# Performance work log

Hardware: AMD Instinct MI355X
Metric: run time of the kernel (lower is better)

Reference implementation:

```python
import jax, jax.numpy as jnp
import numpy as np

D_MODEL = 1024
NUM_HEADS = 16
HEAD_DIM = D_MODEL // NUM_HEADS


def setup_inputs() -> dict:
    key = jax.random.key(0)
    ks = jax.random.split(key, 11)
    B, S, D = 2, 2048, D_MODEL
    scale = 1.0 / np.sqrt(D)
    inp = {
        "query": jax.random.normal(ks[0], (B, S, D), jnp.float32),
        "key": jax.random.normal(ks[1], (B, S, D), jnp.float32),
        "value": jax.random.normal(ks[2], (B, S, D), jnp.float32),
        "Wq": jax.random.normal(ks[3], (D, D), jnp.float32) * scale,
        "bq": jnp.zeros((D,), jnp.float32),
        "Wk": jax.random.normal(ks[4], (D, D), jnp.float32) * scale,
        "bk": jnp.zeros((D,), jnp.float32),
        "Wv": jax.random.normal(ks[5], (D, D), jnp.float32) * scale,
        "bv": jnp.zeros((D,), jnp.float32),
        "Wo": jax.random.normal(ks[6], (D, D), jnp.float32) * scale,
        "bo": jnp.zeros((D,), jnp.float32),
    }
    return inp


def reference(query, key, value, Wq, bq, Wk, bk, Wv, bv, Wo, bo):
    B, S, D = query.shape
    H, hd = NUM_HEADS, HEAD_DIM
    # linear projections (x @ W^T + b, torch nn.Linear convention)
    Q = query @ Wq.T + bq
    K = key @ Wk.T + bk
    V = value @ Wv.T + bv
    # split heads: [B, S, H, hd] -> [B, H, S, hd]
    Q = Q.reshape(B, S, H, hd).transpose(0, 2, 1, 3)
    K = K.reshape(B, S, H, hd).transpose(0, 2, 1, 3)
    V = V.reshape(B, S, H, hd).transpose(0, 2, 1, 3)
    # scaled dot-product attention (explicit, non-flash)
    scores = jnp.einsum("bhqd,bhkd->bhqk", Q, K) / jnp.sqrt(jnp.float32(hd)).astype(Q.dtype)
    attn = jax.nn.softmax(scores, axis=-1)
    out = jnp.einsum("bhqk,bhkd->bhqd", attn, V)
    # merge heads: [B, H, S, hd] -> [B, S, D]
    out = out.transpose(0, 2, 1, 3).reshape(B, S, D)
    return out @ Wo.T + bo
```

## Files before the change

### kernel.cpp

```cpp
#include <hip/hip_runtime.h>
#include <hip/hip_bf16.h>


constexpr int D_MODEL = 1024;
constexpr int S_LEN   = 2048;
constexpr int BATCH   = 2;
constexpr int NH      = 16;
constexpr int HD      = 64;
constexpr int ROWS    = BATCH * S_LEN;

typedef __attribute__((ext_vector_type(8))) short short8;
typedef __attribute__((ext_vector_type(4))) float float4a;

static __device__ __forceinline__ unsigned short f2bf(float f) {
  union { float f; unsigned u; } v{f};
  unsigned r = v.u + 0x7FFFu + ((v.u >> 16) & 1u);
  return (unsigned short)(r >> 16);
}

static __device__ __forceinline__ unsigned pack_bf16(float a, float b) {
#if __has_builtin(__builtin_amdgcn_cvt_pk_bf16_f32)
  typedef __attribute__((ext_vector_type(2))) __bf16 bf16x2;
  union { bf16x2 v; unsigned u; } c;
  c.v = __builtin_amdgcn_cvt_pk_bf16_f32(a, b);
  return c.u;
#else
  return (unsigned)f2bf(a) | ((unsigned)f2bf(b) << 16);
#endif
}

static __device__ __forceinline__ float bf2f(unsigned short u) {
  union { unsigned u; float f; } v;
  v.u = (unsigned)u << 16;
  return v.f;
}

static __device__ __forceinline__ void async16(const void* g, void* l) {
  __builtin_amdgcn_global_load_lds(
      (const __attribute__((address_space(1))) unsigned int*)g,
      (__attribute__((address_space(3))) unsigned int*)l, 16, 0, 0);
}

struct ConvArgs { const float* s[7]; unsigned short* d[7]; int n[7]; };

__global__ __launch_bounds__(256) void convert_bf16(ConvArgs a) {
  const int which = blockIdx.y;
  const int i = (blockIdx.x * 256 + threadIdx.x) * 8;
  if (i >= a.n[which]) return;
  const float4* s = (const float4*)(a.s[which] + i);
  float4 x = s[0], y = s[1];
  unsigned t[4] = {pack_bf16(x.x, x.y), pack_bf16(x.z, x.w),
                   pack_bf16(y.x, y.y), pack_bf16(y.z, y.w)};
  *(short8*)(a.d[which] + i) = *(short8*)t;
}

template <int MODE>
static __device__ __forceinline__ void gemm_body(
    const unsigned short* __restrict__ A, const unsigned short* __restrict__ W,
    const float* __restrict__ bias, void* __restrict__ Yv, float scale,
    unsigned short* As, unsigned short* Bs, unsigned short* Tb) {
  const int tid = threadIdx.x;
  const int w = tid >> 6, lane = tid & 63;
  const int l15 = lane & 15, quad = lane >> 4;
  const int row0 = blockIdx.x * 128, col0 = blockIdx.y * 128;
  const int wm = (w & 1) * 64, wn = (w >> 1) * 64;

  float4a acc[4][4];
#pragma unroll
  for (int i = 0; i < 4; i++)
#pragma unroll
    for (int j = 0; j < 4; j++) acc[i][j] = (float4a){0.f, 0.f, 0.f, 0.f};

  for (int kt = 0; kt < D_MODEL; kt += 64) {
    __syncthreads();
#pragma unroll
    for (int j = 0; j < 4; j++) {
      const int i = w * 4 + j;
      const int r = i * 8 + (lane >> 3);
      const int c = ((lane & 7) - (r >> 1)) & 7;
      async16(W + (size_t)(col0 + r) * D_MODEL + kt + c * 8, (char*)Bs + i * 1024);
      async16(A + (size_t)(row0 + r) * D_MODEL + kt + c * 8, (char*)As + i * 1024);
    }
    __syncthreads();

#pragma unroll
    for (int kk = 0; kk < 2; kk++) {
      const int sw = (kk * 4 + quad + (l15 >> 1)) & 7;
      short8 af[4], bf[4];
#pragma unroll
      for (int mt = 0; mt < 4; mt++) {
        const int r = wm + mt * 16 + l15;
        af[mt] = *(const short8*)&As[(r * 8 + sw) * 8];
      }
#pragma unroll
      for (int nt = 0; nt < 4; nt++) {
        const int r = wn + nt * 16 + l15;
        bf[nt] = *(const short8*)&Bs[(r * 8 + sw) * 8];
      }
#pragma unroll
      for (int mt = 0; mt < 4; mt++)
#pragma unroll
        for (int nt = 0; nt < 4; nt++)
          acc[mt][nt] = __builtin_amdgcn_mfma_f32_16x16x32_bf16(af[mt], bf[nt], acc[mt][nt], 0, 0, 0);
    }
  }

  int cols[4];
  float bvs[4];
#pragma unroll
  for (int nt = 0; nt < 4; nt++) {
    cols[nt] = col0 + wn + nt * 16 + l15;
    bvs[nt]  = bias[cols[nt]] * ((MODE == 0) ? scale : 1.0f);
  }

  if constexpr (MODE == 0) {
    unsigned short* Y = (unsigned short*)Yv;
#pragma unroll
    for (int mt = 0; mt < 4; mt++)
#pragma unroll
      for (int r = 0; r < 4; r++) {
        const int m = row0 + wm + mt * 16 + quad * 4 + r;
        const int bb = m >> 11, s = m & 2047;
#pragma unroll
        for (int nt = 0; nt < 4; nt++) {
          const int h = cols[nt] >> 6, d = cols[nt] & 63;
          Y[(((size_t)(bb * NH + h)) * S_LEN + s) * HD + d] =
              f2bf(acc[mt][nt][r] * scale + bvs[nt]);
        }
      }
  } else {
    __syncthreads();
    unsigned short* T = Tb + w * (64 * 32);
    unsigned short* Y = (unsigned short*)Yv;
#pragma unroll
    for (int p = 0; p < 2; p++) {
      if (p) { asm volatile("s_waitcnt lgkmcnt(0)" ::: "memory"); }
#pragma unroll
      for (int mi = 0; mi < 2; mi++) {
        const int mt = 2 * p + mi;
#pragma unroll
        for (int r = 0; r < 4; r++) {
          const int sl = mi * 16 + quad * 4 + r;
          const int cch = sl >> 3;
#pragma unroll
          for (int nt = 0; nt < 4; nt++) {
            const int dl = nt * 16 + l15;
            const int slot = cch ^ (dl & 3);
            T[dl * 32 + slot * 8 + (sl & 7)] = f2bf(acc[mt][nt][r] + bvs[nt]);
          }
        }
      }
      asm volatile("s_waitcnt lgkmcnt(0)" ::: "memory");
#pragma unroll
      for (int j = 0; j < 4; j++) {
        const int cid = j * 64 + lane;
        const int dl = cid >> 2;
        const int c  = cid & 3;
        const int slot = c ^ (dl & 3);
        short8 v = *(const short8*)&T[dl * 32 + slot * 8];
        const int col = col0 + wn + dl;
        const int h = col >> 6, d = col & 63;
        const int m = row0 + wm + p * 32 + c * 8;
        const int bb = m >> 11, s = m & 2047;
        *(short8*)&Y[(((size_t)(bb * NH + h)) * HD + d) * S_LEN + s] = v;
      }
    }
  }
}

__global__ __launch_bounds__(256) void gemm_qkv(
    const unsigned short* xq, const unsigned short* xk, const unsigned short* xv,
    const unsigned short* wq, const unsigned short* wk, const unsigned short* wv,
    const float* bq, const float* bk, const float* bv,
    unsigned short* Q, unsigned short* K, unsigned short* Vt) {
  __shared__ unsigned short smem[2 * 128 * 64];
  unsigned short* As = smem;
  unsigned short* Bs = smem + 128 * 64;
  unsigned short* Tb = smem;
  const int z = blockIdx.z;
  if (z == 0)      gemm_body<0>(xq, wq, bq, Q,  0.125f * 1.44269504f, As, Bs, Tb);
  else if (z == 1) gemm_body<0>(xk, wk, bk, K,  1.0f, As, Bs, Tb);
  else             gemm_body<2>(xv, wv, bv, Vt, 1.0f, As, Bs, Tb);
}

__global__ __launch_bounds__(256) void gemm_o(
    const unsigned short* __restrict__ Op, const float* __restrict__ Lp,
    const unsigned short* __restrict__ wo, const float* __restrict__ bo,
    float* __restrict__ out) {
  __shared__ unsigned short As[64 * 64];
  __shared__ unsigned short Bs[128 * 64];
  const int tid = threadIdx.x;
  const int w = tid >> 6, lane = tid & 63;
  const int l15 = lane & 15, quad = lane >> 4;
  const int row0 = blockIdx.x * 64, col0 = blockIdx.y * 128;
  const int wn = w * 32;

  const int ar = w * 16 + (lane >> 2);
  const int cg = lane & 3;
  const int asl0 = (cg + (ar >> 1)) & 7;
  const int asl1 = (cg + 4 + (ar >> 1)) & 7;
  const int grow = row0 + ar;
  const unsigned short* P0 = Op + (size_t)grow * D_MODEL + cg * 8;
  const unsigned short* P1 = P0 + (size_t)ROWS * D_MODEL;
  const float* L0 = Lp + (size_t)grow * NH;
  const float* L1 = L0 + (size_t)ROWS * NH;

  float4a acc[4][2];
#pragma unroll
  for (int i = 0; i < 4; i++)
#pragma unroll
    for (int j = 0; j < 2; j++) acc[i][j] = (float4a){0.f, 0.f, 0.f, 0.f};

  for (int kt = 0; kt < D_MODEL; kt += 64) {
    const int h = kt >> 6;
    const float rinv = 1.0f / (L0[h] + L1[h]);
    short8 a0 = *(const short8*)(P0 + kt);
    short8 a1 = *(const short8*)(P0 + kt + 32);
    short8 b0 = *(const short8*)(P1 + kt);
    short8 b1 = *(const short8*)(P1 + kt + 32);
    unsigned t0[4], t1[4];
#pragma unroll
    for (int i = 0; i < 4; i++) {
      const float u0 = (bf2f((unsigned short)a0[2 * i]) + bf2f((unsigned short)b0[2 * i])) * rinv;
      const float u1 = (bf2f((unsigned short)a0[2 * i + 1]) + bf2f((unsigned short)b0[2 * i + 1])) * rinv;
      t0[i] = pack_bf16(u0, u1);
      const float v0 = (bf2f((unsigned short)a1[2 * i]) + bf2f((unsigned short)b1[2 * i])) * rinv;
      const float v1 = (bf2f((unsigned short)a1[2 * i + 1]) + bf2f((unsigned short)b1[2 * i + 1])) * rinv;
      t1[i] = pack_bf16(v0, v1);
    }
    __syncthreads();
    *(short8*)&As[(ar * 8 + asl0) * 8] = *(short8*)t0;
    *(short8*)&As[(ar * 8 + asl1) * 8] = *(short8*)t1;
#pragma unroll
    for (int j = 0; j < 4; j++) {
      const int i = w * 4 + j;
      const int r = i * 8 + (lane >> 3);
      const int c = ((lane & 7) - (r >> 1)) & 7;
      async16(wo + (size_t)(col0 + r) * D_MODEL + kt + c * 8, (char*)Bs + i * 1024);
    }
    __syncthreads();

#pragma unroll
    for (int kk = 0; kk < 2; kk++) {
      const int sw = (kk * 4 + quad + (l15 >> 1)) & 7;
      short8 af[4], bf[2];
#pragma unroll
      for (int mt = 0; mt < 4; mt++) {
        const int r = mt * 16 + l15;
        af[mt] = *(const short8*)&As[(r * 8 + sw) * 8];
      }
#pragma unroll
      for (int nt = 0; nt < 2; nt++) {
        const int r = wn + nt * 16 + l15;
        bf[nt] = *(const short8*)&Bs[(r * 8 + sw) * 8];
      }
#pragma unroll
      for (int mt = 0; mt < 4; mt++)
#pragma unroll
        for (int nt = 0; nt < 2; nt++)
          acc[mt][nt] = __builtin_amdgcn_mfma_f32_16x16x32_bf16(af[mt], bf[nt], acc[mt][nt], 0, 0, 0);
    }
  }

#pragma unroll
  for (int nt = 0; nt < 2; nt++) {
    const int col = col0 + wn + nt * 16 + l15;
    const float bv = bo[col];
#pragma unroll
    for (int mt = 0; mt < 4; mt++)
#pragma unroll
      for (int r = 0; r < 4; r++) {
        const int m = row0 + mt * 16 + quad * 4 + r;
        out[(size_t)m * D_MODEL + col] = acc[mt][nt][r] + bv;
      }
  }
}

__global__ __launch_bounds__(256) void attn_kernel(
    const unsigned short* __restrict__ Qh, const unsigned short* __restrict__ Kh,
    const unsigned short* __restrict__ Vt, unsigned short* __restrict__ Op,
    float* __restrict__ Lp) {
  const int n   = blockIdx.x;
  const int idx = n >> 3;
  const int qb  = idx & 15;
  const int g   = (n & 7) + 8 * (idx >> 4);
  const int h   = g & 15;
  const int z   = g >> 4;
  const int bb  = z >> 1, sp = z & 1;

  const int tid = threadIdx.x;
  const int w = tid >> 6, lane = tid & 63;
  const int l15 = lane & 15, quad = lane >> 4;

  __shared__ unsigned short Ks[64 * 64];
  __shared__ unsigned short Vs[64 * 64];
  __shared__ unsigned short Ps[4][32][72];

  const size_t bh = (size_t)(bb * NH + h);
  const unsigned short* Qp = Qh + bh * S_LEN * HD;
  const unsigned short* Kp = Kh + bh * S_LEN * HD;
  const unsigned short* Vp = Vt + bh * (size_t)HD * S_LEN;

  const int r0 = w * 16 + (lane >> 3);
  const int c0 = ((lane & 7) - r0) & 7;
  const unsigned short* Kg0 = Kp + (size_t)r0 * HD + c0 * 8;
  const unsigned short* Kg1 = Kg0 + 8 * HD;
  const unsigned short* Vg0 = Vp + (size_t)r0 * S_LEN + c0 * 8;
  const unsigned short* Vg1 = Vg0 + 8 * S_LEN;
  unsigned short* Kd0 = (unsigned short*)((char*)Ks + (w * 2) * 1024 + (size_t)lane * 16);
  unsigned short* Kd1 = (unsigned short*)((char*)Kd0 + 1024);
  unsigned short* Vd0 = (unsigned short*)((char*)Vs + (w * 2) * 1024 + (size_t)lane * 16);
  unsigned short* Vd1 = (unsigned short*)((char*)Vd0 + 1024);

  short8 qf[2][2];
#pragma unroll
  for (int qnt = 0; qnt < 2; qnt++)
#pragma unroll
    for (int c = 0; c < 2; c++)
      qf[qnt][c] = *(const short8*)(Qp + (size_t)(qb * 128 + w * 32 + qnt * 16 + l15) * HD +
                                    c * 32 + quad * 8);

  unsigned short ob[8] = {0x3F80, 0x3F80, 0x3F80, 0x3F80, 0x3F80, 0x3F80, 0x3F80, 0x3F80};
  const short8 ones = *(short8*)ob;

  float4a Oacc[2][4];
#pragma unroll
  for (int a = 0; a < 2; a++)
#pragma unroll
    for (int b = 0; b < 4; b++) Oacc[a][b] = (float4a){0.f, 0.f, 0.f, 0.f};
  float4a Lacc[2] = {(float4a){0.f, 0.f, 0.f, 0.f}, (float4a){0.f, 0.f, 0.f, 0.f}};

  const int sw0 = (quad + l15) & 7;
  const int sw1 = (quad + 4 + l15) & 7;

  const int kb0 = sp * 1024, kbend = kb0 + 1024;

  short8 kr0 = *(const short8*)(Kg0 + (size_t)kb0 * HD);
  short8 kr1 = *(const short8*)(Kg1 + (size_t)kb0 * HD);
  short8 vr0 = *(const short8*)(Vg0 + kb0);
  short8 vr1 = *(const short8*)(Vg1 + kb0);

  for (int kb = kb0; kb < kbend; kb += 64) {
    asm volatile("s_waitcnt lgkmcnt(0)" ::: "memory");
    __builtin_amdgcn_sched_barrier(0);
    __builtin_amdgcn_s_barrier();
    asm volatile("s_waitcnt vmcnt(0)" ::: "memory");
    __builtin_amdgcn_sched_barrier(0);
    *(short8*)Kd0 = kr0;
    *(short8*)Kd1 = kr1;
    *(short8*)Vd0 = vr0;
    *(short8*)Vd1 = vr1;
    if (kb + 64 < kbend) {
      kr0 = *(const short8*)(Kg0 + (size_t)(kb + 64) * HD);
      kr1 = *(const short8*)(Kg1 + (size_t)(kb + 64) * HD);
      vr0 = *(const short8*)(Vg0 + (kb + 64));
      vr1 = *(const short8*)(Vg1 + (kb + 64));
    }
    asm volatile("s_waitcnt lgkmcnt(0)" ::: "memory");
    __builtin_amdgcn_sched_barrier(0);
    __builtin_amdgcn_s_barrier();

#pragma unroll
    for (int mt = 0; mt < 4; mt++) {
      const int rb = (mt * 16 + l15) * 8;
      short8 a0 = *(const short8*)&Ks[(rb + sw0) * 8];
      short8 a1 = *(const short8*)&Ks[(rb + sw1) * 8];
#pragma unroll
      for (int qnt = 0; qnt < 2; qnt++) {
        float4a s = (float4a){0.f, 0.f, 0.f, 0.f};
        s = __builtin_amdgcn_mfma_f32_16x16x32_bf16(a0, qf[qnt][0], s, 0, 0, 0);
        s = __builtin_amdgcn_mfma_f32_16x16x32_bf16(a1, qf[qnt][1], s, 0, 0, 0);
        uint2 pk;
        pk.x = pack_bf16(__builtin_amdgcn_exp2f(s[0]), __builtin_amdgcn_exp2f(s[1]));
        pk.y = pack_bf16(__builtin_amdgcn_exp2f(s[2]), __builtin_amdgcn_exp2f(s[3]));
        *(uint2*)&Ps[w][qnt * 16 + l15][mt * 16 + quad * 4] = pk;
      }
    }
    asm volatile("s_waitcnt lgkmcnt(0)" ::: "memory");

#pragma unroll
    for (int c = 0; c < 2; c++) {
      short8 pa0 = *(const short8*)&Ps[w][l15][c * 32 + quad * 8];
      short8 pa1 = *(const short8*)&Ps[w][16 + l15][c * 32 + quad * 8];
      Lacc[0] = __builtin_amdgcn_mfma_f32_16x16x32_bf16(pa0, ones, Lacc[0], 0, 0, 0);
      Lacc[1] = __builtin_amdgcn_mfma_f32_16x16x32_bf16(pa1, ones, Lacc[1], 0, 0, 0);
      const int vsw = (c * 4 + quad + l15) & 7;
#pragma unroll
      for (int nt = 0; nt < 4; nt++) {
        short8 vb = *(const short8*)&Vs[((nt * 16 + l15) * 8 + vsw) * 8];
        Oacc[0][nt] = __builtin_amdgcn_mfma_f32_16x16x32_bf16(pa0, vb, Oacc[0][nt], 0, 0, 0);
        Oacc[1][nt] = __builtin_amdgcn_mfma_f32_16x16x32_bf16(pa1, vb, Oacc[1][nt], 0, 0, 0);
      }
    }
  }

  if (l15 == 0) {
#pragma unroll
    for (int qnt = 0; qnt < 2; qnt++)
#pragma unroll
      for (int reg = 0; reg < 4; reg++) {
        const int q = qb * 128 + w * 32 + qnt * 16 + quad * 4 + reg;
        Lp[(size_t)sp * ROWS * NH + ((size_t)bb * S_LEN + q) * NH + h] = Lacc[qnt][reg];
      }
  }

  unsigned short* Ob = Op + (size_t)sp * ROWS * D_MODEL;
#pragma unroll
  for (int qnt = 0; qnt < 2; qnt++) {
#pragma unroll
    for (int reg = 0; reg < 4; reg++) {
      const int q = qb * 128 + w * 32 + qnt * 16 + quad * 4 + reg;
      unsigned short* orow = Ob + ((size_t)bb * S_LEN + q) * D_MODEL + h * HD;
#pragma unroll
      for (int nt = 0; nt < 4; nt++)
        orow[nt * 16 + l15] = f2bf(Oacc[qnt][nt][reg]);
    }
  }
}

extern "C" void kernel_launch(void* const* d_in, const int* in_sizes, int n_in,
                              void* d_out, int out_size, void* d_ws, size_t ws_size,
                              hipStream_t stream) {
  const float* query = (const float*)d_in[0];
  const float* key   = (const float*)d_in[1];
  const float* value = (const float*)d_in[2];
  const float* Wq = (const float*)d_in[3];
  const float* bq = (const float*)d_in[4];
  const float* Wk = (const float*)d_in[5];
  const float* bk = (const float*)d_in[6];
  const float* Wv = (const float*)d_in[7];
  const float* bv = (const float*)d_in[8];
  const float* Wo = (const float*)d_in[9];
  const float* bo = (const float*)d_in[10];
  float* out = (float*)d_out;

  char* ws = (char*)d_ws;
  const size_t MB = 1024 * 1024;
  unsigned short* xq16 = (unsigned short*)(ws + 0 * MB);
  unsigned short* xk16 = (unsigned short*)(ws + 8 * MB);
  unsigned short* xv16 = (unsigned short*)(ws + 16 * MB);
  unsigned short* wq16 = (unsigned short*)(ws + 24 * MB);
  unsigned short* wk16 = (unsigned short*)(ws + 26 * MB);
  unsigned short* wv16 = (unsigned short*)(ws + 28 * MB);
  unsigned short* qbuf  = (unsigned short*)(ws + 32 * MB);
  unsigned short* kbuf  = (unsigned short*)(ws + 40 * MB);
  unsigned short* vtbuf = (unsigned short*)(ws + 48 * MB);
  unsigned short* wo16  = (unsigned short*)(ws + 56 * MB);
  float* Lp = (float*)(ws + 58 * MB);
  unsigned short* Op = (unsigned short*)(ws + 0 * MB);

  ConvArgs ca;
  const int NX = ROWS * D_MODEL, NW = D_MODEL * D_MODEL;
  ca.s[0] = query; ca.d[0] = xq16; ca.n[0] = NX;
  ca.s[1] = key;   ca.d[1] = xk16; ca.n[1] = NX;
  ca.s[2] = value; ca.d[2] = xv16; ca.n[2] = NX;
  ca.s[3] = Wq;    ca.d[3] = wq16; ca.n[3] = NW;
  ca.s[4] = Wk;    ca.d[4] = wk16; ca.n[4] = NW;
  ca.s[5] = Wv;    ca.d[5] = wv16; ca.n[5] = NW;
  ca.s[6] = Wo;    ca.d[6] = wo16; ca.n[6] = NW;
  hipLaunchKernelGGL(convert_bf16, dim3(NX / 2048, 7), dim3(256), 0, stream, ca);

  dim3 gqkv(ROWS / 128, D_MODEL / 128, 3);
  hipLaunchKernelGGL(gemm_qkv, gqkv, dim3(256), 0, stream,
                     xq16, xk16, xv16, wq16, wk16, wv16, bq, bk, bv,
                     qbuf, kbuf, vtbuf);

  hipLaunchKernelGGL(attn_kernel, dim3(1024), dim3(256), 0, stream,
                     qbuf, kbuf, vtbuf, Op, Lp);

  dim3 go(ROWS / 64, D_MODEL / 128);
  hipLaunchKernelGGL(gemm_o, go, dim3(256), 0, stream, Op, Lp, wo16, bo, out);
}
```

Before: 232.3 us.

## Fuse activation fp32-to-bf16 conversion into QKV GEMM and double-buffer weight tiles

The QKV GEMM now reads fp32 activations directly, converts them to bf16 in registers and writes them to LDS, so the separate conversion pass over the three activation tensors and its round trip through memory are gone. Weight tiles in both the QKV and output GEMMs are double-buffered in LDS, with the next tile's async loads issued before the MFMAs of the current tile. This uses more LDS and registers (prefetched fp32 A values), which may lower occupancy, and each QKV block now reads twice as many activation bytes as the bf16 version did.

```diff
diff --git a/kernel.cpp b/kernel.cpp
--- a/kernel.cpp
+++ b/kernel.cpp
@@ -41,7 +41,17 @@
       (__attribute__((address_space(3))) unsigned int*)l, 16, 0, 0);
 }
 
-struct ConvArgs { const float* s[7]; unsigned short* d[7]; int n[7]; };
+#define WAIT_LGKM0_SB() do { \
+  asm volatile("s_waitcnt lgkmcnt(0)" ::: "memory"); \
+  __builtin_amdgcn_sched_barrier(0); } while (0)
+#define WAIT_VM0_SB() do { \
+  asm volatile("s_waitcnt vmcnt(0)" ::: "memory"); \
+  __builtin_amdgcn_sched_barrier(0); } while (0)
+#define BARRIER_SB() do { \
+  __builtin_amdgcn_s_barrier(); \
+  __builtin_amdgcn_sched_barrier(0); } while (0)
+
+struct ConvArgs { const float* s[4]; unsigned short* d[4]; int n[4]; };
 
 __global__ __launch_bounds__(256) void convert_bf16(ConvArgs a) {
   const int which = blockIdx.y;
@@ -56,32 +66,69 @@
 
 template <int MODE>
 static __device__ __forceinline__ void gemm_body(
-    const unsigned short* __restrict__ A, const unsigned short* __restrict__ W,
+    const float* __restrict__ A, const unsigned short* __restrict__ W,
     const float* __restrict__ bias, void* __restrict__ Yv, float scale,
-    unsigned short* As, unsigned short* Bs, unsigned short* Tb) {
+    unsigned short* As, unsigned short* Bsb, unsigned short* Tb) {
   const int tid = threadIdx.x;
   const int w = tid >> 6, lane = tid & 63;
   const int l15 = lane & 15, quad = lane >> 4;
   const int row0 = blockIdx.x * 128, col0 = blockIdx.y * 128;
   const int wm = (w & 1) * 64, wn = (w >> 1) * 64;
 
-  float4a acc[4][4];
-#pragma unroll
-  for (int i = 0; i < 4; i++)
-#pragma unroll
-    for (int j = 0; j < 4; j++) acc[i][j] = (float4a){0.f, 0.f, 0.f, 0.f};
-
-  for (int kt = 0; kt < D_MODEL; kt += 64) {
-    __syncthreads();
+  int rA[4], cA[4];
+#pragma unroll
+  for (int j = 0; j < 4; j++) {
+    const int i = w * 4 + j;
+    rA[j] = i * 8 + (lane >> 3);
+    cA[j] = ((lane & 7) - (rA[j] >> 1)) & 7;
+  }
+
+  float4 av[4][2];
+  auto loadA = [&](int kt) {
+#pragma unroll
+    for (int j = 0; j < 4; j++) {
+      const float* s = A + (size_t)(row0 + rA[j]) * D_MODEL + kt + cA[j] * 8;
+      av[j][0] = *(const float4*)s;
+      av[j][1] = *(const float4*)(s + 4);
+    }
+  };
+  auto loadW = [&](int kt, unsigned short* Bdst) {
 #pragma unroll
     for (int j = 0; j < 4; j++) {
       const int i = w * 4 + j;
-      const int r = i * 8 + (lane >> 3);
-      const int c = ((lane & 7) - (r >> 1)) & 7;
-      async16(W + (size_t)(col0 + r) * D_MODEL + kt + c * 8, (char*)Bs + i * 1024);
-      async16(A + (size_t)(row0 + r) * D_MODEL + kt + c * 8, (char*)As + i * 1024);
-    }
-    __syncthreads();
+      async16(W + (size_t)(col0 + rA[j]) * D_MODEL + kt + cA[j] * 8,
+              (char*)Bdst + i * 1024);
+    }
+  };
+
+  float4a acc[4][4];
+#pragma unroll
+  for (int i = 0; i < 4; i++)
+#pragma unroll
+    for (int j = 0; j < 4; j++) acc[i][j] = (float4a){0.f, 0.f, 0.f, 0.f};
+
+  loadA(0);
+  loadW(0, Bsb);
+
+  for (int kt = 0; kt < D_MODEL; kt += 64) {
+    const int cur = (kt >> 6) & 1;
+    unsigned short* Bc = Bsb + cur * (128 * 64);
+    unsigned short* Bn = Bsb + (cur ^ 1) * (128 * 64);
+    const bool more = (kt + 64 < D_MODEL);
+
+    WAIT_LGKM0_SB();
+    BARRIER_SB();
+    WAIT_VM0_SB();
+#pragma unroll
+    for (int j = 0; j < 4; j++) {
+      unsigned t[4] = {pack_bf16(av[j][0].x, av[j][0].y), pack_bf16(av[j][0].z, av[j][0].w),
+                       pack_bf16(av[j][1].x, av[j][1].y), pack_bf16(av[j][1].z, av[j][1].w)};
+      *(short8*)((char*)As + (w * 4 + j) * 1024 + (size_t)lane * 16) = *(short8*)t;
+    }
+    if (more) loadA(kt + 64);
+    WAIT_LGKM0_SB();
+    BARRIER_SB();
+    if (more) loadW(kt + 64, Bn);
 
 #pragma unroll
     for (int kk = 0; kk < 2; kk++) {
@@ -95,7 +142,7 @@
 #pragma unroll
       for (int nt = 0; nt < 4; nt++) {
         const int r = wn + nt * 16 + l15;
-        bf[nt] = *(const short8*)&Bs[(r * 8 + sw) * 8];
+        bf[nt] = *(const short8*)&Bc[(r * 8 + sw) * 8];
       }
 #pragma unroll
       for (int mt = 0; mt < 4; mt++)
@@ -169,18 +216,18 @@
 }
 
 __global__ __launch_bounds__(256) void gemm_qkv(
-    const unsigned short* xq, const unsigned short* xk, const unsigned short* xv,
+    const float* xq, const float* xk, const float* xv,
     const unsigned short* wq, const unsigned short* wk, const unsigned short* wv,
     const float* bq, const float* bk, const float* bv,
     unsigned short* Q, unsigned short* K, unsigned short* Vt) {
-  __shared__ unsigned short smem[2 * 128 * 64];
-  unsigned short* As = smem;
-  unsigned short* Bs = smem + 128 * 64;
-  unsigned short* Tb = smem;
+  __shared__ unsigned short smem[3 * 128 * 64];
+  unsigned short* As  = smem;
+  unsigned short* Bsb = smem + 128 * 64;
+  unsigned short* Tb  = smem;
   const int z = blockIdx.z;
-  if (z == 0)      gemm_body<0>(xq, wq, bq, Q,  0.125f * 1.44269504f, As, Bs, Tb);
-  else if (z == 1) gemm_body<0>(xk, wk, bk, K,  1.0f, As, Bs, Tb);
-  else             gemm_body<2>(xv, wv, bv, Vt, 1.0f, As, Bs, Tb);
+  if (z == 0)      gemm_body<0>(xq, wq, bq, Q,  0.125f * 1.44269504f, As, Bsb, Tb);
+  else if (z == 1) gemm_body<0>(xk, wk, bk, K,  1.0f, As, Bsb, Tb);
+  else             gemm_body<2>(xv, wv, bv, Vt, 1.0f, As, Bsb, Tb);
 }
 
 __global__ __launch_bounds__(256) void gemm_o(
@@ -188,7 +235,7 @@
     const unsigned short* __restrict__ wo, const float* __restrict__ bo,
     float* __restrict__ out) {
   __shared__ unsigned short As[64 * 64];
-  __shared__ unsigned short Bs[128 * 64];
+  __shared__ unsigned short Bsb[2 * 128 * 64];
   const int tid = threadIdx.x;
   const int w = tid >> 6, lane = tid & 63;
   const int l15 = lane & 15, quad = lane >> 4;
@@ -205,40 +252,71 @@
   const float* L0 = Lp + (size_t)grow * NH;
   const float* L1 = L0 + (size_t)ROWS * NH;
 
-  float4a acc[4][2];
-#pragma unroll
-  for (int i = 0; i < 4; i++)
-#pragma unroll
-    for (int j = 0; j < 2; j++) acc[i][j] = (float4a){0.f, 0.f, 0.f, 0.f};
-
-  for (int kt = 0; kt < D_MODEL; kt += 64) {
-    const int h = kt >> 6;
-    const float rinv = 1.0f / (L0[h] + L1[h]);
-    short8 a0 = *(const short8*)(P0 + kt);
-    short8 a1 = *(const short8*)(P0 + kt + 32);
-    short8 b0 = *(const short8*)(P1 + kt);
-    short8 b1 = *(const short8*)(P1 + kt + 32);
-    unsigned t0[4], t1[4];
-#pragma unroll
-    for (int i = 0; i < 4; i++) {
-      const float u0 = (bf2f((unsigned short)a0[2 * i]) + bf2f((unsigned short)b0[2 * i])) * rinv;
-      const float u1 = (bf2f((unsigned short)a0[2 * i + 1]) + bf2f((unsigned short)b0[2 * i + 1])) * rinv;
-      t0[i] = pack_bf16(u0, u1);
-      const float v0 = (bf2f((unsigned short)a1[2 * i]) + bf2f((unsigned short)b1[2 * i])) * rinv;
-      const float v1 = (bf2f((unsigned short)a1[2 * i + 1]) + bf2f((unsigned short)b1[2 * i + 1])) * rinv;
-      t1[i] = pack_bf16(v0, v1);
-    }
-    __syncthreads();
-    *(short8*)&As[(ar * 8 + asl0) * 8] = *(short8*)t0;
-    *(short8*)&As[(ar * 8 + asl1) * 8] = *(short8*)t1;
+  int rB[4], cB[4];
+#pragma unroll
+  for (int j = 0; j < 4; j++) {
+    const int i = w * 4 + j;
+    rB[j] = i * 8 + (lane >> 3);
+    cB[j] = ((lane & 7) - (rB[j] >> 1)) & 7;
+  }
+  auto loadW = [&](int kt, unsigned short* Bdst) {
 #pragma unroll
     for (int j = 0; j < 4; j++) {
       const int i = w * 4 + j;
-      const int r = i * 8 + (lane >> 3);
-      const int c = ((lane & 7) - (r >> 1)) & 7;
-      async16(wo + (size_t)(col0 + r) * D_MODEL + kt + c * 8, (char*)Bs + i * 1024);
-    }
-    __syncthreads();
+      async16(wo + (size_t)(col0 + rB[j]) * D_MODEL + kt + cB[j] * 8,
+              (char*)Bdst + i * 1024);
+    }
+  };
+
+  float4a acc[4][2];
+#pragma unroll
+  for (int i = 0; i < 4; i++)
+#pragma unroll
+    for (int j = 0; j < 2; j++) acc[i][j] = (float4a){0.f, 0.f, 0.f, 0.f};
+
+  short8 a0 = *(const short8*)(P0 + 0);
+  short8 a1 = *(const short8*)(P0 + 32);
+  short8 b0 = *(const short8*)(P1 + 0);
+  short8 b1 = *(const short8*)(P1 + 32);
+  float l0r = L0[0], l1r = L1[0];
+  loadW(0, Bsb);
+
+  for (int kt = 0; kt < D_MODEL; kt += 64) {
+    const int cur = (kt >> 6) & 1;
+    unsigned short* Bc = Bsb + cur * (128 * 64);
+    unsigned short* Bn = Bsb + (cur ^ 1) * (128 * 64);
+    const bool more = (kt + 64 < D_MODEL);
+
+    WAIT_LGKM0_SB();
+    BARRIER_SB();
+    WAIT_VM0_SB();
+    {
+      const float rinv = 1.0f / (l0r + l1r);
+      unsigned t0[4], t1[4];
+#pragma unroll
+      for (int i = 0; i < 4; i++) {
+        const float u0 = (bf2f((unsigned short)a0[2 * i]) + bf2f((unsigned short)b0[2 * i])) * rinv;
+        const float u1 = (bf2f((unsigned short)a0[2 * i + 1]) + bf2f((unsigned short)b0[2 * i + 1])) * rinv;
+        t0[i] = pack_bf16(u0, u1);
+        const float v0 = (bf2f((unsigned short)a1[2 * i]) + bf2f((unsigned short)b1[2 * i])) * rinv;
+        const float v1 = (bf2f((unsigned short)a1[2 * i + 1]) + bf2f((unsigned short)b1[2 * i + 1])) * rinv;
+        t1[i] = pack_bf16(v0, v1);
+      }
+      *(short8*)&As[(ar * 8 + asl0) * 8] = *(short8*)t0;
+      *(short8*)&As[(ar * 8 + asl1) * 8] = *(short8*)t1;
+    }
+    if (more) {
+      const int ktn = kt + 64, hn = ktn >> 6;
+      a0 = *(const short8*)(P0 + ktn);
+      a1 = *(const short8*)(P0 + ktn + 32);
+      b0 = *(const short8*)(P1 + ktn);
+      b1 = *(const short8*)(P1 + ktn + 32);
+      l0r = L0[hn];
+      l1r = L1[hn];
+    }
+    WAIT_LGKM0_SB();
+    BARRIER_SB();
+    if (more) loadW(kt + 64, Bn);
 
 #pragma unroll
     for (int kk = 0; kk < 2; kk++) {
@@ -252,7 +330,7 @@
 #pragma unroll
       for (int nt = 0; nt < 2; nt++) {
         const int r = wn + nt * 16 + l15;
-        bf[nt] = *(const short8*)&Bs[(r * 8 + sw) * 8];
+        bf[nt] = *(const short8*)&Bc[(r * 8 + sw) * 8];
       }
 #pragma unroll
       for (int mt = 0; mt < 4; mt++)
@@ -436,9 +514,6 @@
 
   char* ws = (char*)d_ws;
   const size_t MB = 1024 * 1024;
-  unsigned short* xq16 = (unsigned short*)(ws + 0 * MB);
-  unsigned short* xk16 = (unsigned short*)(ws + 8 * MB);
-  unsigned short* xv16 = (unsigned short*)(ws + 16 * MB);
   unsigned short* wq16 = (unsigned short*)(ws + 24 * MB);
   unsigned short* wk16 = (unsigned short*)(ws + 26 * MB);
   unsigned short* wv16 = (unsigned short*)(ws + 28 * MB);
@@ -450,19 +525,16 @@
   unsigned short* Op = (unsigned short*)(ws + 0 * MB);
 
   ConvArgs ca;
-  const int NX = ROWS * D_MODEL, NW = D_MODEL * D_MODEL;
-  ca.s[0] = query; ca.d[0] = xq16; ca.n[0] = NX;
-  ca.s[1] = key;   ca.d[1] = xk16; ca.n[1] = NX;
-  ca.s[2] = value; ca.d[2] = xv16; ca.n[2] = NX;
-  ca.s[3] = Wq;    ca.d[3] = wq16; ca.n[3] = NW;
-  ca.s[4] = Wk;    ca.d[4] = wk16; ca.n[4] = NW;
-  ca.s[5] = Wv;    ca.d[5] = wv16; ca.n[5] = NW;
-  ca.s[6] = Wo;    ca.d[6] = wo16; ca.n[6] = NW;
-  hipLaunchKernelGGL(convert_bf16, dim3(NX / 2048, 7), dim3(256), 0, stream, ca);
+  const int NW = D_MODEL * D_MODEL;
+  ca.s[0] = Wq; ca.d[0] = wq16; ca.n[0] = NW;
+  ca.s[1] = Wk; ca.d[1] = wk16; ca.n[1] = NW;
+  ca.s[2] = Wv; ca.d[2] = wv16; ca.n[2] = NW;
+  ca.s[3] = Wo; ca.d[3] = wo16; ca.n[3] = NW;
+  hipLaunchKernelGGL(convert_bf16, dim3(NW / 2048, 4), dim3(256), 0, stream, ca);
 
   dim3 gqkv(ROWS / 128, D_MODEL / 128, 3);
   hipLaunchKernelGGL(gemm_qkv, gqkv, dim3(256), 0, stream,
-                     xq16, xk16, xv16, wq16, wk16, wv16, bq, bk, bv,
+                     query, key, value, wq16, wk16, wv16, bq, bk, bv,
                      qbuf, kbuf, vtbuf);
 
   hipLaunchKernelGGL(attn_kernel, dim3(1024), dim3(256), 0, stream,
```

New measurement: 232.0 us. Within noise of the previous version (-0.1%).
